# Performance work log

Hardware: AMD Instinct MI355X
Metric: run time of the kernel (lower is better)

## Reference

```python
import jax, jax.numpy as jnp
import numpy as np
import math

B, S, IN_DIM = 2048, 60, 211
D, H, L, DFF, NC = 192, 6, 3, 768, 35
DK = D // H


def make_pe(seq_len, d_model):
    pos = np.arange(seq_len)[:, None].astype(np.float32)
    div = np.exp(np.arange(0, d_model, 2).astype(np.float32) * (-math.log(10000.0) / d_model))
    pe = np.zeros((seq_len, d_model), dtype=np.float32)
    pe[:, 0::2] = np.sin(pos * div)
    pe[:, 1::2] = np.cos(pos * div)
    return jnp.asarray(pe)


def setup_inputs() -> dict:
    key = jax.random.key(0)
    ks = jax.random.split(key, 24)
    r = lambda k, shape, fan: jax.random.normal(k, shape, jnp.float32) * (1.0 / np.sqrt(fan))
    inp = {
        'x': jax.random.normal(ks[0], (B, S, IN_DIM), jnp.float32),
        'W_in': r(ks[1], (IN_DIM, D), IN_DIM), 'b_in': jnp.zeros((D,), jnp.float32),
        'pe': make_pe(S, D),
        'Wq': r(ks[2], (L, D, D), D), 'bq': jnp.zeros((L, D), jnp.float32),
        'Wk': r(ks[3], (L, D, D), D), 'bk': jnp.zeros((L, D), jnp.float32),
        'Wv': r(ks[4], (L, D, D), D), 'bv': jnp.zeros((L, D), jnp.float32),
        'Wo': r(ks[5], (L, D, D), D), 'bo': jnp.zeros((L, D), jnp.float32),
        'W1': r(ks[6], (L, D, DFF), D), 'b1': jnp.zeros((L, DFF), jnp.float32),
        'W2': r(ks[7], (L, DFF, D), DFF), 'b2': jnp.zeros((L, D), jnp.float32),
        'g1': jnp.ones((L, D), jnp.float32), 'be1': jnp.zeros((L, D), jnp.float32),
        'g2': jnp.ones((L, D), jnp.float32), 'be2': jnp.zeros((L, D), jnp.float32),
        'Wc1': r(ks[8], (D, D // 2), D), 'bc1': jnp.zeros((D // 2,), jnp.float32),
        'Wc2': r(ks[9], (D // 2, NC), D // 2), 'bc2': jnp.zeros((NC,), jnp.float32),
    }
    return inp


def layer_norm(x, g, b, eps=1e-5):
    mu = jnp.mean(x, axis=-1, keepdims=True)
    var = jnp.mean((x - mu) ** 2, axis=-1, keepdims=True)
    return (x - mu) * jax.lax.rsqrt(var + eps) * g + b


def mha(x, Wq, bq, Wk, bk, Wv, bv, Wo, bo):
    Bs, Ss, _ = x.shape
    q = (x @ Wq + bq).reshape(Bs, Ss, H, DK)
    k = (x @ Wk + bk).reshape(Bs, Ss, H, DK)
    v = (x @ Wv + bv).reshape(Bs, Ss, H, DK)
    scores = jnp.einsum('bqhd,bkhd->bhqk', q, k) / jnp.sqrt(jnp.float32(DK))
    attn = jax.nn.softmax(scores, axis=-1)
    ctx = jnp.einsum('bhqk,bkhd->bqhd', attn, v).reshape(Bs, Ss, D)
    return ctx @ Wo + bo


def encoder_layer(x, Wq, bq, Wk, bk, Wv, bv, Wo, bo, W1, b1, W2, b2, g1, be1, g2, be2):
    attn_out = mha(x, Wq, bq, Wk, bk, Wv, bv, Wo, bo)
    x = layer_norm(x + attn_out, g1, be1)
    ff = jax.nn.gelu(x @ W1 + b1, approximate=False) @ W2 + b2
    return layer_norm(x + ff, g2, be2)


def reference(x, W_in, b_in, pe, Wq, bq, Wk, bk, Wv, bv, Wo, bo,
              W1, b1, W2, b2, g1, be1, g2, be2, Wc1, bc1, Wc2, bc2):
    h = x @ W_in + b_in + pe  # [B,S,D]
    for l in range(L):
        h = encoder_layer(h, Wq[l], bq[l], Wk[l], bk[l], Wv[l], bv[l], Wo[l], bo[l],
                          W1[l], b1[l], W2[l], b2[l], g1[l], be1[l], g2[l], be2[l])
    hidden = jax.nn.gelu(h @ Wc1 + bc1, approximate=False)
    return hidden @ Wc2 + bc2  # [B,S,NC]
```

## Files before the change

kernel.cpp:

```cpp
#include <hip/hip_runtime.h>
#include <cmath>

#define B_   2048
#define S_   60
#define NTOK (B_*S_)
#define IND_ 211
#define D_   192
#define H_   6
#define DK_  32
#define L_   3
#define DFF_ 768
#define NC_  35
#define DH_  96

typedef unsigned short us_t;
typedef us_t us8 __attribute__((ext_vector_type(8)));
typedef us_t us4 __attribute__((ext_vector_type(4)));
typedef short sh8 __attribute__((ext_vector_type(8)));
typedef float f4 __attribute__((ext_vector_type(4)));

#define MFMA(a, b, cc) __builtin_amdgcn_mfma_f32_16x16x32_bf16((a), (b), (cc), 0, 0, 0)
#define ZACC(A, M, N) \
    for (int _i = 0; _i < (M); ++_i) \
        for (int _j = 0; _j < (N); ++_j) { \
            A[_i][_j][0] = 0.f; A[_i][_j][1] = 0.f; A[_i][_j][2] = 0.f; A[_i][_j][3] = 0.f; }
#define ZACC1(A, N) \
    for (int _j = 0; _j < (N); ++_j) { \
        A[_j][0] = 0.f; A[_j][1] = 0.f; A[_j][2] = 0.f; A[_j][3] = 0.f; }

__device__ __forceinline__ float bf2f(us_t u) {
    union { unsigned int i; float f; } v; v.i = ((unsigned int)u) << 16; return v.f;
}
__device__ __forceinline__ us_t f2bf(float f) {
    union { float f; unsigned int i; } v; v.f = f;
    unsigned int r = v.i + 0x7fffu + ((v.i >> 16) & 1u);
    return (us_t)(r >> 16);
}
__device__ __forceinline__ float gelu_f(float v) {
    float u = v * (0.7978845608f + 0.0356774081f * v * v);
    float e = __expf(2.f * u);
    float t = 1.f - 2.f / (e + 1.f);
    return 0.5f * v * (1.f + t);
}
__device__ __forceinline__ void gld16(const us_t* g, us_t* s) {
    __builtin_amdgcn_global_load_lds(
        (const __attribute__((address_space(1))) unsigned int*)(g),
        (__attribute__((address_space(3))) unsigned int*)(s), 16, 0, 0);
}

__global__ void prep_t(const float* __restrict__ in, us_t* __restrict__ out,
                       int K, int Kpad, int N)
{
    int e = blockIdx.x * 256 + threadIdx.x;
    if (e >= N * Kpad) return;
    int n = e / Kpad, kp = e % Kpad;
    out[e] = (kp < K) ? f2bf(in[(size_t)kp * N + n]) : (us_t)0;
}

__global__ void prep_ff(const float* __restrict__ W1, const float* __restrict__ W2,
                        us_t* __restrict__ WT)
{
    int e = blockIdx.x * 256 + threadIdx.x;
    if (e >= L_ * 48 * 6144) return;
    int l = e / (48 * 6144), r = e % (48 * 6144);
    int t = r / 6144, q = r % 6144;
    int col = q >> 5, kk = q & 31;
    int cb = t / 12, ph = (t / 6) & 1, s = t % 6;
    us_t v;
    if (!ph) v = f2bf(W1[((size_t)l * D_ + s * 32 + kk) * DFF_ + cb * 192 + col]);
    else     v = f2bf(W2[((size_t)l * DFF_ + cb * 192 + s * 32 + kk) * D_ + col]);
    WT[e] = v;
}

__global__ __launch_bounds__(256) void inp_mfma(
    const float* __restrict__ x, const us_t* __restrict__ Wint,
    const float* __restrict__ b_in, const float* __restrict__ pe,
    us_t* __restrict__ h)
{
    __shared__ __align__(16) char smem[29696 + 27648];
    us_t* Xs = (us_t*)smem;
    us_t* Ws = (us_t*)(smem + 29696);
    const int tid = threadIdx.x;
    const int lane = tid & 63, wid = tid >> 6;
    const int g = lane >> 4, c = lane & 15;
    const int wr = wid >> 1, wc = wid & 1;
    const int row0 = blockIdx.x * 64;

    for (int e = tid; e < 64 * 224; e += 256) {
        int tok = e / 224, kp = e % 224;
        float v = (kp < IND_) ? x[(size_t)(row0 + tok) * IND_ + kp] : 0.f;
        Xs[tok * 232 + kp] = f2bf(v);
    }

    f4 acc[2][6];
    ZACC(acc, 2, 6);
    for (int pc = 0; pc < 4; ++pc) {
        __syncthreads();
        const int nk = (pc < 3) ? 64 : 32;
        const int per = nk / 8;
        for (int e = tid; e < 192 * per; e += 256) {
            int rw = e / per, v = e % per;
            *(us8*)&Ws[rw * 72 + v * 8] =
                *(const us8*)&Wint[(size_t)rw * 224 + pc * 64 + v * 8];
        }
        __syncthreads();
        for (int kk = 0; kk < nk / 32; ++kk) {
            const int ka = pc * 64 + kk * 32 + g * 8;
            const int kw = kk * 32 + g * 8;
            sh8 a0 = *(const sh8*)&Xs[(32 * wr + c) * 232 + ka];
            sh8 a1 = *(const sh8*)&Xs[(32 * wr + 16 + c) * 232 + ka];
            #pragma unroll
            for (int ni = 0; ni < 6; ++ni) {
                sh8 bf = *(const sh8*)&Ws[(96 * wc + 16 * ni + c) * 72 + kw];
                acc[0][ni] = MFMA(a0, bf, acc[0][ni]);
                acc[1][ni] = MFMA(a1, bf, acc[1][ni]);
            }
        }
    }
    #pragma unroll
    for (int ni = 0; ni < 6; ++ni) {
        const int col = 96 * wc + 16 * ni + c;
        const float bv = b_in[col];
        #pragma unroll
        for (int mi = 0; mi < 2; ++mi)
            #pragma unroll
            for (int r = 0; r < 4; ++r) {
                int tokg = row0 + 32 * wr + 16 * mi + 4 * g + r;
                int s = tokg % S_;
                float val = acc[mi][ni][r] + bv + pe[(size_t)s * D_ + col];
                h[(size_t)tokg * D_ + col] = f2bf(val);
            }
    }
}

__global__ __launch_bounds__(512) void qkv_attn_wo(
    us_t* __restrict__ h,
    const us_t* __restrict__ Wqt, const us_t* __restrict__ Wkt,
    const us_t* __restrict__ Wvt, const us_t* __restrict__ Wot,
    const float* __restrict__ bq, const float* __restrict__ bk,
    const float* __restrict__ bv, const float* __restrict__ bo,
    const float* __restrict__ g1, const float* __restrict__ be1)
{
    __shared__ __align__(16) char smem[157696];
    us_t* Xs = (us_t*)smem;
    us_t* Qs = (us_t*)(smem + 25600);
    us_t* Ks = (us_t*)(smem + 51200);
    us_t* Vt = (us_t*)(smem + 76800);
    us_t* Ws = (us_t*)(smem + 104448);
    us_t* P0 = (us_t*)(smem + 104448);
    us_t* P1 = (us_t*)(smem + 113664);
    us_t* Cx = (us_t*)(smem + 132096);
    float* eL = (float*)(smem + 51200);

    const int tid = threadIdx.x;
    const int lane = tid & 63, wid = tid >> 6;
    const int g = lane >> 4, c = lane & 15;
    const int wr = wid >> 2, wc = wid & 3;
    us_t* hb = h + (size_t)blockIdx.x * (S_ * D_);

    for (int e = tid; e < 1536; e += 512) {
        int tok = e / 24, v = e % 24;
        us8 u = {0, 0, 0, 0, 0, 0, 0, 0};
        if (tok < S_) u = *(const us8*)&hb[(size_t)tok * D_ + v * 8];
        *(us8*)&Xs[tok * 200 + v * 8] = u;
    }

    for (int m = 0; m < 3; ++m) {
        const us_t* Wt = (m == 0) ? Wqt : (m == 1) ? Wkt : Wvt;
        const float* bb = (m == 0) ? bq : (m == 1) ? bk : bv;
        f4 acc[2][3];
        ZACC(acc, 2, 3);
        for (int pc = 0; pc < 3; ++pc) {
            __syncthreads();
            for (int e = tid; e < 1536; e += 512) {
                int rw = e >> 3, v = e & 7;
                *(us8*)&Ws[rw * 72 + v * 8] =
                    *(const us8*)&Wt[(size_t)rw * 192 + pc * 64 + v * 8];
            }
            __syncthreads();
            #pragma unroll
            for (int kk = 0; kk < 2; ++kk) {
                const int ka = pc * 64 + kk * 32 + g * 8;
                const int kw = kk * 32 + g * 8;
                sh8 a0 = *(const sh8*)&Xs[(32 * wr + c) * 200 + ka];
                sh8 a1 = *(const sh8*)&Xs[(32 * wr + 16 + c) * 200 + ka];
                #pragma unroll
                for (int ni = 0; ni < 3; ++ni) {
                    sh8 bf = *(const sh8*)&Ws[(48 * wc + 16 * ni + c) * 72 + kw];
                    acc[0][ni] = MFMA(a0, bf, acc[0][ni]);
                    acc[1][ni] = MFMA(a1, bf, acc[1][ni]);
                }
            }
        }
        #pragma unroll
        for (int ni = 0; ni < 3; ++ni) {
            const int col = 48 * wc + 16 * ni + c;
            const float bval = bb[col];
            #pragma unroll
            for (int mi = 0; mi < 2; ++mi)
                #pragma unroll
                for (int r = 0; r < 4; ++r) {
                    int tok = 32 * wr + 16 * mi + 4 * g + r;
                    us_t o = f2bf(acc[mi][ni][r] + bval);
                    if (m == 0)      Qs[tok * 200 + col] = o;
                    else if (m == 1) Ks[tok * 200 + col] = o;
                    else             Vt[col * 72 + tok] = o;
                }
        }
    }
    __syncthreads();

    const int hgrp = wid & 3;
    const int hsel = wid >> 2;
    for (int rr = 0; rr < 3; ++rr) {
        const int hh = 2 * rr + hsel;
        us_t* Pb = hsel ? P1 : P0;
        f4 sc[4];
        ZACC1(sc, 4);
        {
            const int ka = 32 * hh + g * 8;
            sh8 aq = *(const sh8*)&Qs[(16 * hgrp + c) * 200 + ka];
            #pragma unroll
            for (int ni = 0; ni < 4; ++ni) {
                sh8 bk8 = *(const sh8*)&Ks[(16 * ni + c) * 200 + ka];
                sc[ni] = MFMA(aq, bk8, sc[ni]);
            }
        }
        #pragma unroll
        for (int r = 0; r < 4; ++r) {
            float mx = -1e30f;
            #pragma unroll
            for (int ni = 0; ni < 4; ++ni) {
                float v = sc[ni][r] * 0.17677669529663687f;
                if (16 * ni + c >= S_) v = -1e30f;
                sc[ni][r] = v;
                mx = fmaxf(mx, v);
            }
            mx = fmaxf(mx, __shfl_xor(mx, 1));
            mx = fmaxf(mx, __shfl_xor(mx, 2));
            mx = fmaxf(mx, __shfl_xor(mx, 4));
            mx = fmaxf(mx, __shfl_xor(mx, 8));
            float sum = 0.f;
            #pragma unroll
            for (int ni = 0; ni < 4; ++ni) {
                float e = __expf(sc[ni][r] - mx);
                sc[ni][r] = e; sum += e;
            }
            sum += __shfl_xor(sum, 1);
            sum += __shfl_xor(sum, 2);
            sum += __shfl_xor(sum, 4);
            sum += __shfl_xor(sum, 8);
            const float inv = 1.f / sum;
            #pragma unroll
            for (int ni = 0; ni < 4; ++ni)
                Pb[(16 * hgrp + 4 * g + r) * 72 + 16 * ni + c] = f2bf(sc[ni][r] * inv);
        }
        __syncthreads();
        f4 ov[2];
        ZACC1(ov, 2);
        #pragma unroll
        for (int kk = 0; kk < 2; ++kk) {
            sh8 ap = *(const sh8*)&Pb[(16 * hgrp + c) * 72 + kk * 32 + g * 8];
            #pragma unroll
            for (int n2 = 0; n2 < 2; ++n2) {
                sh8 bv8 = *(const sh8*)&Vt[(32 * hh + 16 * n2 + c) * 72 + kk * 32 + g * 8];
                ov[n2] = MFMA(ap, bv8, ov[n2]);
            }
        }
        #pragma unroll
        for (int n2 = 0; n2 < 2; ++n2)
            #pragma unroll
            for (int r = 0; r < 4; ++r)
                Cx[(16 * hgrp + 4 * g + r) * 200 + 32 * hh + 16 * n2 + c] = f2bf(ov[n2][r]);
        __syncthreads();
    }

    f4 aw[2][3];
    ZACC(aw, 2, 3);
    for (int pc = 0; pc < 3; ++pc) {
        __syncthreads();
        for (int e = tid; e < 1536; e += 512) {
            int rw = e >> 3, v = e & 7;
            *(us8*)&Ws[rw * 72 + v * 8] =
                *(const us8*)&Wot[(size_t)rw * 192 + pc * 64 + v * 8];
        }
        __syncthreads();
        #pragma unroll
        for (int kk = 0; kk < 2; ++kk) {
            const int ka = pc * 64 + kk * 32 + g * 8;
            const int kw = kk * 32 + g * 8;
            sh8 a0 = *(const sh8*)&Cx[(32 * wr + c) * 200 + ka];
            sh8 a1 = *(const sh8*)&Cx[(32 * wr + 16 + c) * 200 + ka];
            #pragma unroll
            for (int ni = 0; ni < 3; ++ni) {
                sh8 bf = *(const sh8*)&Ws[(48 * wc + 16 * ni + c) * 72 + kw];
                aw[0][ni] = MFMA(a0, bf, aw[0][ni]);
                aw[1][ni] = MFMA(a1, bf, aw[1][ni]);
            }
        }
    }
    __syncthreads();
    #pragma unroll
    for (int ni = 0; ni < 3; ++ni) {
        const int col = 48 * wc + 16 * ni + c;
        const float bov = bo[col];
        #pragma unroll
        for (int mi = 0; mi < 2; ++mi)
            #pragma unroll
            for (int r = 0; r < 4; ++r) {
                int tok = 32 * wr + 16 * mi + 4 * g + r;
                eL[tok * 200 + col] = aw[mi][ni][r] + bov + bf2f(Xs[tok * 200 + col]);
            }
    }
    __syncthreads();
    {
        const int tok = tid >> 3, t8 = tid & 7;
        float vals[24], sum = 0.f, ssq = 0.f;
        #pragma unroll
        for (int jv = 0; jv < 6; ++jv) {
            float4 v4 = *(const float4*)&eL[tok * 200 + t8 * 24 + jv * 4];
            vals[jv*4+0] = v4.x; vals[jv*4+1] = v4.y; vals[jv*4+2] = v4.z; vals[jv*4+3] = v4.w;
            sum += v4.x + v4.y + v4.z + v4.w;
            ssq += v4.x*v4.x + v4.y*v4.y + v4.z*v4.z + v4.w*v4.w;
        }
        sum += __shfl_xor(sum, 1); sum += __shfl_xor(sum, 2); sum += __shfl_xor(sum, 4);
        ssq += __shfl_xor(ssq, 1); ssq += __shfl_xor(ssq, 2); ssq += __shfl_xor(ssq, 4);
        const float mean = sum * (1.f / D_);
        const float var  = ssq * (1.f / D_) - mean * mean;
        const float rstd = rsqrtf(var + 1e-5f);
        if (tok < S_) {
            #pragma unroll
            for (int jv = 0; jv < 6; ++jv) {
                us4 o4;
                #pragma unroll
                for (int j = 0; j < 4; ++j) {
                    int col = t8 * 24 + jv * 4 + j;
                    o4[j] = f2bf((vals[jv*4+j] - mean) * rstd * g1[col] + be1[col]);
                }
                *(us4*)&hb[(size_t)tok * D_ + t8 * 24 + jv * 4] = o4;
            }
        }
    }
}

__global__ __launch_bounds__(512) void ff_mfma(
    us_t* __restrict__ hio,
    const us_t* __restrict__ WT, const float* __restrict__ b1,
    const float* __restrict__ b2,
    const float* __restrict__ gamma, const float* __restrict__ beta)
{
    __shared__ __align__(16) char smem[76800];
    us_t* Xs  = (us_t*)smem;
    us_t* Ts  = (us_t*)(smem + 25600);
    us_t* Wsb = (us_t*)(smem + 51200);
    float* Sm = (float*)(smem + 75776);

    const int tid = threadIdx.x;
    const int lane = tid & 63, wid = tid >> 6;
    const int g = lane >> 4, c = lane & 15;
    const int wr = wid >> 1;
    const int wc = wid & 1;
    const int row0 = blockIdx.x * 64;

    auto stage = [&](int t) {
        const us_t* src = WT + (size_t)t * 6144;
        us_t* dst = Wsb + (t & 1) * 6144;
        for (int i = wid; i < 12; i += 8)
            gld16(src + i * 512 + lane * 8, dst + i * 512);
    };

    for (int e = tid; e < 1536; e += 512) {
        int tok = e / 24, v = e % 24;
        *(us8*)&Xs[tok * 200 + v * 8] = *(const us8*)&hio[(size_t)(row0 + tok) * D_ + v * 8];
    }
    stage(0);
    __syncthreads();

    f4 acc1[6], acc2[6];
    ZACC1(acc2, 6);
    for (int t = 0; t < 48; ++t) {
        const int s = t % 6, ph = (t / 6) & 1, cb = t / 12;
        if (t < 47) stage(t + 1);
        const us_t* W = Wsb + (t & 1) * 6144;
        if (!ph) {
            if (s == 0) ZACC1(acc1, 6);
            sh8 xb = *(const sh8*)&Xs[(16 * wr + c) * 200 + s * 32 + g * 8];
            #pragma unroll
            for (int ni = 0; ni < 6; ++ni) {
                sh8 wa = *(const sh8*)&W[(96 * wc + 16 * ni + c) * 32 + g * 8];
                acc1[ni] = MFMA(wa, xb, acc1[ni]);
            }
            if (s == 5) {
                #pragma unroll
                for (int ni = 0; ni < 6; ++ni) {
                    const int d0 = 96 * wc + 16 * ni + 4 * g;
                    us4 o4;
                    #pragma unroll
                    for (int r = 0; r < 4; ++r)
                        o4[r] = f2bf(gelu_f(acc1[ni][r] + b1[cb * 192 + d0 + r]));
                    *(us4*)&Ts[(16 * wr + c) * 200 + d0] = o4;
                }
            }
        } else {
            sh8 tb = *(const sh8*)&Ts[(16 * wr + c) * 200 + s * 32 + g * 8];
            #pragma unroll
            for (int ni = 0; ni < 6; ++ni) {
                sh8 wa = *(const sh8*)&W[(96 * wc + 16 * ni + c) * 32 + g * 8];
                acc2[ni] = MFMA(wa, tb, acc2[ni]);
            }
        }
        __syncthreads();
    }

    float v[6][4];
    float sum = 0.f, ssq = 0.f;
    const int xrow = (16 * wr + c) * 200;
    #pragma unroll
    for (int ni = 0; ni < 6; ++ni)
        #pragma unroll
        for (int r = 0; r < 4; ++r) {
            const int dcol = 96 * wc + 16 * ni + 4 * g + r;
            float val = acc2[ni][r] + b2[dcol] + bf2f(Xs[xrow + dcol]);
            v[ni][r] = val; sum += val; ssq += val * val;
        }
    sum += __shfl_xor(sum, 16); sum += __shfl_xor(sum, 32);
    ssq += __shfl_xor(ssq, 16); ssq += __shfl_xor(ssq, 32);
    if (g == 0) {
        Sm[((0 * 2 + wc) * 4 + wr) * 16 + c] = sum;
        Sm[((1 * 2 + wc) * 4 + wr) * 16 + c] = ssq;
    }
    __syncthreads();
    sum += Sm[((0 * 2 + (1 - wc)) * 4 + wr) * 16 + c];
    ssq += Sm[((1 * 2 + (1 - wc)) * 4 + wr) * 16 + c];
    const float mean = sum * (1.f / D_);
    const float var  = ssq * (1.f / D_) - mean * mean;
    const float rstd = rsqrtf(var + 1e-5f);
    us_t* orow = hio + (size_t)(row0 + 16 * wr + c) * D_;
    #pragma unroll
    for (int ni = 0; ni < 6; ++ni) {
        const int d0 = 96 * wc + 16 * ni + 4 * g;
        us4 o4;
        #pragma unroll
        for (int r = 0; r < 4; ++r)
            o4[r] = f2bf((v[ni][r] - mean) * rstd * gamma[d0 + r] + beta[d0 + r]);
        *(us4*)&orow[d0] = o4;
    }
}

__global__ __launch_bounds__(256) void clf1_mfma(
    const us_t* __restrict__ h, const us_t* __restrict__ Wc1t,
    const float* __restrict__ bc1, us_t* __restrict__ hid)
{
    __shared__ __align__(16) char smem[25600 + 13824];
    us_t* Xs = (us_t*)smem;
    us_t* Ws = (us_t*)(smem + 25600);
    const int tid = threadIdx.x;
    const int lane = tid & 63, wid = tid >> 6;
    const int g = lane >> 4, c = lane & 15;
    const int wr = wid >> 1, wc = wid & 1;
    const int row0 = blockIdx.x * 64;

    for (int e = tid; e < 1536; e += 256) {
        int tok = e / 24, v = e % 24;
        *(us8*)&Xs[tok * 200 + v * 8] = *(const us8*)&h[(size_t)(row0 + tok) * D_ + v * 8];
    }
    f4 acc[2][3];
    ZACC(acc, 2, 3);
    for (int pc = 0; pc < 3; ++pc) {
        __syncthreads();
        for (int e = tid; e < 768; e += 256) {
            int rw = e >> 3, v = e & 7;
            *(us8*)&Ws[rw * 72 + v * 8] =
                *(const us8*)&Wc1t[(size_t)rw * 192 + pc * 64 + v * 8];
        }
        __syncthreads();
        #pragma unroll
        for (int kk = 0; kk < 2; ++kk) {
            const int ka = pc * 64 + kk * 32 + g * 8;
            const int kw = kk * 32 + g * 8;
            sh8 a0 = *(const sh8*)&Xs[(32 * wr + c) * 200 + ka];
            sh8 a1 = *(const sh8*)&Xs[(32 * wr + 16 + c) * 200 + ka];
            #pragma unroll
            for (int ni = 0; ni < 3; ++ni) {
                sh8 bf = *(const sh8*)&Ws[(48 * wc + 16 * ni + c) * 72 + kw];
                acc[0][ni] = MFMA(a0, bf, acc[0][ni]);
                acc[1][ni] = MFMA(a1, bf, acc[1][ni]);
            }
        }
    }
    #pragma unroll
    for (int ni = 0; ni < 3; ++ni) {
        const int col = 48 * wc + 16 * ni + c;
        const float bv = bc1[col];
        #pragma unroll
        for (int mi = 0; mi < 2; ++mi)
            #pragma unroll
            for (int r = 0; r < 4; ++r) {
                int tok = row0 + 32 * wr + 16 * mi + 4 * g + r;
                hid[(size_t)tok * DH_ + col] = f2bf(gelu_f(acc[mi][ni][r] + bv));
            }
    }
}

__global__ __launch_bounds__(256) void clf2_kernel(
    const us_t* __restrict__ hid, const float* __restrict__ Wc2,
    const float* __restrict__ bc2, float* __restrict__ out)
{
    __shared__ us_t Hs[64 * 104];
    __shared__ float Wl[DH_ * NC_];
    __shared__ float bl[NC_];
    const int tid = threadIdx.x;
    const int row0 = blockIdx.x * 64;
    for (int e = tid; e < 768; e += 256) {
        int tok = e / 12, v = e % 12;
        *(us8*)&Hs[tok * 104 + v * 8] = *(const us8*)&hid[(size_t)(row0 + tok) * DH_ + v * 8];
    }
    for (int e = tid; e < DH_ * NC_; e += 256) Wl[e] = Wc2[e];
    if (tid < NC_) bl[tid] = bc2[tid];
    __syncthreads();
    for (int e = tid; e < 64 * NC_; e += 256) {
        const int tok = e / NC_, col = e % NC_;
        float acc = bl[col];
        #pragma unroll 8
        for (int kk = 0; kk < DH_; ++kk)
            acc = fmaf(bf2f(Hs[tok * 104 + kk]), Wl[kk * NC_ + col], acc);
        out[(size_t)(row0 + tok) * NC_ + col] = acc;
    }
}

extern "C" void kernel_launch(void* const* d_in, const int* in_sizes, int n_in,
                              void* d_out, int out_size, void* d_ws, size_t ws_size,
                              hipStream_t stream)
{
    const float* x    = (const float*)d_in[0];
    const float* W_in = (const float*)d_in[1];
    const float* b_in = (const float*)d_in[2];
    const float* pe   = (const float*)d_in[3];
    const float* Wq   = (const float*)d_in[4];
    const float* bq   = (const float*)d_in[5];
    const float* Wk   = (const float*)d_in[6];
    const float* bk   = (const float*)d_in[7];
    const float* Wv   = (const float*)d_in[8];
    const float* bv   = (const float*)d_in[9];
    const float* Wo   = (const float*)d_in[10];
    const float* bo   = (const float*)d_in[11];
    const float* W1   = (const float*)d_in[12];
    const float* b1   = (const float*)d_in[13];
    const float* W2   = (const float*)d_in[14];
    const float* b2   = (const float*)d_in[15];
    const float* g1   = (const float*)d_in[16];
    const float* be1  = (const float*)d_in[17];
    const float* g2   = (const float*)d_in[18];
    const float* be2  = (const float*)d_in[19];
    const float* Wc1  = (const float*)d_in[20];
    const float* bc1  = (const float*)d_in[21];
    const float* Wc2  = (const float*)d_in[22];
    const float* bc2  = (const float*)d_in[23];
    float* outp = (float*)d_out;

    us_t* h    = (us_t*)d_ws;
    us_t* hid  = h + (size_t)NTOK * D_;
    us_t* Wint = hid + (size_t)NTOK * DH_;
    us_t* Wqt  = Wint + 192 * 224;
    us_t* Wkt  = Wqt + 3 * 36864;
    us_t* Wvt  = Wkt + 3 * 36864;
    us_t* Wot  = Wvt + 3 * 36864;
    us_t* WT   = Wot + 3 * 36864;
    us_t* Wc1t = WT + (size_t)L_ * 48 * 6144;

    prep_t<<<168, 256, 0, stream>>>(W_in, Wint, IND_, 224, D_);
    for (int l = 0; l < L_; ++l) {
        prep_t<<<144, 256, 0, stream>>>(Wq + (size_t)l * 36864, Wqt + (size_t)l * 36864, 192, 192, 192);
        prep_t<<<144, 256, 0, stream>>>(Wk + (size_t)l * 36864, Wkt + (size_t)l * 36864, 192, 192, 192);
        prep_t<<<144, 256, 0, stream>>>(Wv + (size_t)l * 36864, Wvt + (size_t)l * 36864, 192, 192, 192);
        prep_t<<<144, 256, 0, stream>>>(Wo + (size_t)l * 36864, Wot + (size_t)l * 36864, 192, 192, 192);
    }
    prep_ff<<<(L_ * 48 * 6144 + 255) / 256, 256, 0, stream>>>(W1, W2, WT);
    prep_t<<<72, 256, 0, stream>>>(Wc1, Wc1t, 192, 192, DH_);

    inp_mfma<<<NTOK / 64, 256, 0, stream>>>(x, Wint, b_in, pe, h);

    for (int l = 0; l < L_; ++l) {
        qkv_attn_wo<<<B_, 512, 0, stream>>>(
            h,
            Wqt + (size_t)l * 36864, Wkt + (size_t)l * 36864,
            Wvt + (size_t)l * 36864, Wot + (size_t)l * 36864,
            bq + l * D_, bk + l * D_, bv + l * D_, bo + l * D_,
            g1 + l * D_, be1 + l * D_);
        ff_mfma<<<NTOK / 64, 512, 0, stream>>>(
            h, WT + (size_t)l * 48 * 6144, b1 + l * DFF_, b2 + l * D_,
            g2 + l * D_, be2 + l * D_);
    }

    clf1_mfma<<<NTOK / 64, 256, 0, stream>>>(h, Wc1t, bc1, hid);
    clf2_kernel<<<NTOK / 64, 256, 0, stream>>>(hid, Wc2, bc2, outp);
}
```

Before: 1.349 ms.

## Retile FF kernel warps to 2x4 and pad weight tiles to 40-element rows

```diff
diff --git a/kernel.cpp b/kernel.cpp
--- a/kernel.cpp
+++ b/kernel.cpp
@@ -61,14 +61,16 @@
                         us_t* __restrict__ WT)
 {
     int e = blockIdx.x * 256 + threadIdx.x;
-    if (e >= L_ * 48 * 6144) return;
-    int l = e / (48 * 6144), r = e % (48 * 6144);
-    int t = r / 6144, q = r % 6144;
-    int col = q >> 5, kk = q & 31;
+    if (e >= L_ * 48 * 7680) return;
+    int l = e / (48 * 7680), r = e % (48 * 7680);
+    int t = r / 7680, q = r % 7680;
+    int col = q / 40, kk = q % 40;
     int cb = t / 12, ph = (t / 6) & 1, s = t % 6;
-    us_t v;
-    if (!ph) v = f2bf(W1[((size_t)l * D_ + s * 32 + kk) * DFF_ + cb * 192 + col]);
-    else     v = f2bf(W2[((size_t)l * DFF_ + cb * 192 + s * 32 + kk) * D_ + col]);
+    us_t v = 0;
+    if (kk < 32) {
+        if (!ph) v = f2bf(W1[((size_t)l * D_ + s * 32 + kk) * DFF_ + cb * 192 + col]);
+        else     v = f2bf(W2[((size_t)l * DFF_ + cb * 192 + s * 32 + kk) * D_ + col]);
+    }
     WT[e] = v;
 }
 
@@ -349,23 +351,23 @@
     const float* __restrict__ b2,
     const float* __restrict__ gamma, const float* __restrict__ beta)
 {
-    __shared__ __align__(16) char smem[76800];
+    __shared__ __align__(16) char smem[81920];
     us_t* Xs  = (us_t*)smem;
     us_t* Ts  = (us_t*)(smem + 25600);
     us_t* Wsb = (us_t*)(smem + 51200);
-    float* Sm = (float*)(smem + 75776);
+    float* Sm = (float*)(smem + 25600);
 
     const int tid = threadIdx.x;
     const int lane = tid & 63, wid = tid >> 6;
     const int g = lane >> 4, c = lane & 15;
-    const int wr = wid >> 1;
-    const int wc = wid & 1;
+    const int wr = wid >> 2;
+    const int wc = wid & 3;
     const int row0 = blockIdx.x * 64;
 
     auto stage = [&](int t) {
-        const us_t* src = WT + (size_t)t * 6144;
-        us_t* dst = Wsb + (t & 1) * 6144;
-        for (int i = wid; i < 12; i += 8)
+        const us_t* src = WT + (size_t)t * 7680;
+        us_t* dst = Wsb + (t & 1) * 7680;
+        for (int i = wid; i < 15; i += 8)
             gld16(src + i * 512 + lane * 8, dst + i * 512);
     };
 
@@ -376,74 +378,100 @@
     stage(0);
     __syncthreads();
 
-    f4 acc1[6], acc2[6];
-    ZACC1(acc2, 6);
+    f4 acc1[2][3], acc2[2][3];
+    ZACC(acc2, 2, 3);
     for (int t = 0; t < 48; ++t) {
         const int s = t % 6, ph = (t / 6) & 1, cb = t / 12;
         if (t < 47) stage(t + 1);
-        const us_t* W = Wsb + (t & 1) * 6144;
+        const us_t* W = Wsb + (t & 1) * 7680;
         if (!ph) {
-            if (s == 0) ZACC1(acc1, 6);
-            sh8 xb = *(const sh8*)&Xs[(16 * wr + c) * 200 + s * 32 + g * 8];
-            #pragma unroll
-            for (int ni = 0; ni < 6; ++ni) {
-                sh8 wa = *(const sh8*)&W[(96 * wc + 16 * ni + c) * 32 + g * 8];
-                acc1[ni] = MFMA(wa, xb, acc1[ni]);
+            if (s == 0) ZACC(acc1, 2, 3);
+            sh8 xb0 = *(const sh8*)&Xs[(32 * wr + c) * 200 + s * 32 + g * 8];
+            sh8 xb1 = *(const sh8*)&Xs[(32 * wr + 16 + c) * 200 + s * 32 + g * 8];
+            #pragma unroll
+            for (int ni = 0; ni < 3; ++ni) {
+                sh8 wa = *(const sh8*)&W[(48 * wc + 16 * ni + c) * 40 + g * 8];
+                acc1[0][ni] = MFMA(wa, xb0, acc1[0][ni]);
+                acc1[1][ni] = MFMA(wa, xb1, acc1[1][ni]);
             }
             if (s == 5) {
                 #pragma unroll
-                for (int ni = 0; ni < 6; ++ni) {
-                    const int d0 = 96 * wc + 16 * ni + 4 * g;
-                    us4 o4;
+                for (int mi = 0; mi < 2; ++mi)
                     #pragma unroll
-                    for (int r = 0; r < 4; ++r)
-                        o4[r] = f2bf(gelu_f(acc1[ni][r] + b1[cb * 192 + d0 + r]));
-                    *(us4*)&Ts[(16 * wr + c) * 200 + d0] = o4;
-                }
+                    for (int ni = 0; ni < 3; ++ni) {
+                        const int d0 = 48 * wc + 16 * ni + 4 * g;
+                        const int tok = 32 * wr + 16 * mi + c;
+                        us4 o4;
+                        #pragma unroll
+                        for (int r = 0; r < 4; ++r)
+                            o4[r] = f2bf(gelu_f(acc1[mi][ni][r] + b1[cb * 192 + d0 + r]));
+                        *(us4*)&Ts[tok * 200 + d0] = o4;
+                    }
             }
         } else {
-            sh8 tb = *(const sh8*)&Ts[(16 * wr + c) * 200 + s * 32 + g * 8];
-            #pragma unroll
-            for (int ni = 0; ni < 6; ++ni) {
-                sh8 wa = *(const sh8*)&W[(96 * wc + 16 * ni + c) * 32 + g * 8];
-                acc2[ni] = MFMA(wa, tb, acc2[ni]);
-            }
-        }
-        __syncthreads();
-    }
-
-    float v[6][4];
-    float sum = 0.f, ssq = 0.f;
-    const int xrow = (16 * wr + c) * 200;
+            sh8 tb0 = *(const sh8*)&Ts[(32 * wr + c) * 200 + s * 32 + g * 8];
+            sh8 tb1 = *(const sh8*)&Ts[(32 * wr + 16 + c) * 200 + s * 32 + g * 8];
+            #pragma unroll
+            for (int ni = 0; ni < 3; ++ni) {
+                sh8 wa = *(const sh8*)&W[(48 * wc + 16 * ni + c) * 40 + g * 8];
+                acc2[0][ni] = MFMA(wa, tb0, acc2[0][ni]);
+                acc2[1][ni] = MFMA(wa, tb1, acc2[1][ni]);
+            }
+        }
+        __syncthreads();
+    }
+
+    float v[2][3][4];
+    float sum[2] = {0.f, 0.f}, ssq[2] = {0.f, 0.f};
     #pragma unroll
-    for (int ni = 0; ni < 6; ++ni)
-        #pragma unroll
-        for (int r = 0; r < 4; ++r) {
-            const int dcol = 96 * wc + 16 * ni + 4 * g + r;
-            float val = acc2[ni][r] + b2[dcol] + bf2f(Xs[xrow + dcol]);
-            v[ni][r] = val; sum += val; ssq += val * val;
-        }
-    sum += __shfl_xor(sum, 16); sum += __shfl_xor(sum, 32);
-    ssq += __shfl_xor(ssq, 16); ssq += __shfl_xor(ssq, 32);
+    for (int mi = 0; mi < 2; ++mi) {
+        const int tok = 32 * wr + 16 * mi + c;
+        #pragma unroll
+        for (int ni = 0; ni < 3; ++ni) {
+            const int d0 = 48 * wc + 16 * ni + 4 * g;
+            us4 rv = *(const us4*)&Xs[tok * 200 + d0];
+            #pragma unroll
+            for (int r = 0; r < 4; ++r) {
+                float val = acc2[mi][ni][r] + b2[d0 + r] + bf2f(rv[r]);
+                v[mi][ni][r] = val; sum[mi] += val; ssq[mi] += val * val;
+            }
+        }
+    }
+    #pragma unroll
+    for (int mi = 0; mi < 2; ++mi) {
+        sum[mi] += __shfl_xor(sum[mi], 16); sum[mi] += __shfl_xor(sum[mi], 32);
+        ssq[mi] += __shfl_xor(ssq[mi], 16); ssq[mi] += __shfl_xor(ssq[mi], 32);
+    }
     if (g == 0) {
-        Sm[((0 * 2 + wc) * 4 + wr) * 16 + c] = sum;
-        Sm[((1 * 2 + wc) * 4 + wr) * 16 + c] = ssq;
+        #pragma unroll
+        for (int mi = 0; mi < 2; ++mi) {
+            Sm[(((0 * 4 + wc) * 2 + wr) * 2 + mi) * 16 + c] = sum[mi];
+            Sm[(((1 * 4 + wc) * 2 + wr) * 2 + mi) * 16 + c] = ssq[mi];
+        }
     }
     __syncthreads();
-    sum += Sm[((0 * 2 + (1 - wc)) * 4 + wr) * 16 + c];
-    ssq += Sm[((1 * 2 + (1 - wc)) * 4 + wr) * 16 + c];
-    const float mean = sum * (1.f / D_);
-    const float var  = ssq * (1.f / D_) - mean * mean;
-    const float rstd = rsqrtf(var + 1e-5f);
-    us_t* orow = hio + (size_t)(row0 + 16 * wr + c) * D_;
     #pragma unroll
-    for (int ni = 0; ni < 6; ++ni) {
-        const int d0 = 96 * wc + 16 * ni + 4 * g;
-        us4 o4;
-        #pragma unroll
-        for (int r = 0; r < 4; ++r)
-            o4[r] = f2bf((v[ni][r] - mean) * rstd * gamma[d0 + r] + beta[d0 + r]);
-        *(us4*)&orow[d0] = o4;
+    for (int mi = 0; mi < 2; ++mi) {
+        float st = 0.f, qt = 0.f;
+        #pragma unroll
+        for (int w = 0; w < 4; ++w) {
+            st += Sm[(((0 * 4 + w) * 2 + wr) * 2 + mi) * 16 + c];
+            qt += Sm[(((1 * 4 + w) * 2 + wr) * 2 + mi) * 16 + c];
+        }
+        const float mean = st * (1.f / D_);
+        const float var  = qt * (1.f / D_) - mean * mean;
+        const float rstd = rsqrtf(var + 1e-5f);
+        const int tok = 32 * wr + 16 * mi + c;
+        us_t* orow = hio + (size_t)(row0 + tok) * D_;
+        #pragma unroll
+        for (int ni = 0; ni < 3; ++ni) {
+            const int d0 = 48 * wc + 16 * ni + 4 * g;
+            us4 o4;
+            #pragma unroll
+            for (int r = 0; r < 4; ++r)
+                o4[r] = f2bf((v[mi][ni][r] - mean) * rstd * gamma[d0 + r] + beta[d0 + r]);
+            *(us4*)&orow[d0] = o4;
+        }
     }
 }
 
@@ -566,7 +594,7 @@
     us_t* Wvt  = Wkt + 3 * 36864;
     us_t* Wot  = Wvt + 3 * 36864;
     us_t* WT   = Wot + 3 * 36864;
-    us_t* Wc1t = WT + (size_t)L_ * 48 * 6144;
+    us_t* Wc1t = WT + (size_t)L_ * 48 * 7680;
 
     prep_t<<<168, 256, 0, stream>>>(W_in, Wint, IND_, 224, D_);
     for (int l = 0; l < L_; ++l) {
@@ -575,7 +603,7 @@
         prep_t<<<144, 256, 0, stream>>>(Wv + (size_t)l * 36864, Wvt + (size_t)l * 36864, 192, 192, 192);
         prep_t<<<144, 256, 0, stream>>>(Wo + (size_t)l * 36864, Wot + (size_t)l * 36864, 192, 192, 192);
     }
-    prep_ff<<<(L_ * 48 * 6144 + 255) / 256, 256, 0, stream>>>(W1, W2, WT);
+    prep_ff<<<(L_ * 48 * 7680 + 255) / 256, 256, 0, stream>>>(W1, W2, WT);
     prep_t<<<72, 256, 0, stream>>>(Wc1, Wc1t, 192, 192, DH_);
 
     inp_mfma<<<NTOK / 64, 256, 0, stream>>>(x, Wint, b_in, pe, h);
@@ -588,7 +616,7 @@
             bq + l * D_, bk + l * D_, bv + l * D_, bo + l * D_,
             g1 + l * D_, be1 + l * D_);
         ff_mfma<<<NTOK / 64, 512, 0, stream>>>(
-            h, WT + (size_t)l * 48 * 6144, b1 + l * DFF_, b2 + l * D_,
+            h, WT + (size_t)l * 48 * 7680, b1 + l * DFF_, b2 + l * D_,
             g2 + l * D_, be2 + l * D_);
     }
 
```

New measurement: 1.265 ms. -6.2%, faster.

## Restructure FFN kernel to keep activations in registers with triple-buffered padded weights

Applied to the files above, without the earlier changes.

```diff
diff --git a/kernel.cpp b/kernel.cpp
--- a/kernel.cpp
+++ b/kernel.cpp
@@ -18,6 +18,7 @@
 typedef us_t us4 __attribute__((ext_vector_type(4)));
 typedef short sh8 __attribute__((ext_vector_type(8)));
 typedef float f4 __attribute__((ext_vector_type(4)));
+typedef int i4v __attribute__((ext_vector_type(4)));
 
 #define MFMA(a, b, cc) __builtin_amdgcn_mfma_f32_16x16x32_bf16((a), (b), (cc), 0, 0, 0)
 #define ZACC(A, M, N) \
@@ -61,14 +62,18 @@
                         us_t* __restrict__ WT)
 {
     int e = blockIdx.x * 256 + threadIdx.x;
-    if (e >= L_ * 48 * 6144) return;
-    int l = e / (48 * 6144), r = e % (48 * 6144);
-    int t = r / 6144, q = r % 6144;
-    int col = q >> 5, kk = q & 31;
-    int cb = t / 12, ph = (t / 6) & 1, s = t % 6;
-    us_t v;
-    if (!ph) v = f2bf(W1[((size_t)l * D_ + s * 32 + kk) * DFF_ + cb * 192 + col]);
-    else     v = f2bf(W2[((size_t)l * DFF_ + cb * 192 + s * 32 + kk) * D_ + col]);
+    if (e >= L_ * 48 * 8192) return;
+    int l = e / (48 * 8192), r = e % (48 * 8192);
+    int t = r / 8192, q = r % 8192;
+    int cb = t / 12, p = t % 12, ph = p / 6, s = p % 6;
+    us_t v = 0;
+    if (q < 7680) {
+        int col = q / 40, kk = q % 40;
+        if (kk < 32) {
+            if (!ph) v = f2bf(W1[((size_t)l * D_ + s * 32 + kk) * DFF_ + cb * 192 + col]);
+            else     v = f2bf(W2[((size_t)l * DFF_ + cb * 192 + s * 32 + kk) * D_ + col]);
+        }
+    }
     WT[e] = v;
 }
 
@@ -349,100 +354,132 @@
     const float* __restrict__ b2,
     const float* __restrict__ gamma, const float* __restrict__ beta)
 {
-    __shared__ __align__(16) char smem[76800];
-    us_t* Xs  = (us_t*)smem;
-    us_t* Ts  = (us_t*)(smem + 25600);
-    us_t* Wsb = (us_t*)(smem + 51200);
-    float* Sm = (float*)(smem + 75776);
+    __shared__ __align__(16) us_t Wsb[3][8192];
 
     const int tid = threadIdx.x;
     const int lane = tid & 63, wid = tid >> 6;
     const int g = lane >> 4, c = lane & 15;
-    const int wr = wid >> 1;
-    const int wc = wid & 1;
-    const int row0 = blockIdx.x * 64;
-
-    auto stage = [&](int t) {
-        const us_t* src = WT + (size_t)t * 6144;
-        us_t* dst = Wsb + (t & 1) * 6144;
-        for (int i = wid; i < 12; i += 8)
-            gld16(src + i * 512 + lane * 8, dst + i * 512);
+    const int row0 = blockIdx.x * 128;
+    const int trow = row0 + 16 * wid + c;
+
+    auto stage = [&](int t, int slot) {
+        const us_t* src = WT + (size_t)t * 8192;
+        us_t* dst = &Wsb[slot][0];
+        #pragma unroll
+        for (int i = 0; i < 2; ++i)
+            gld16(src + (wid * 2 + i) * 512 + lane * 8, dst + (wid * 2 + i) * 512);
     };
 
-    for (int e = tid; e < 1536; e += 512) {
-        int tok = e / 24, v = e % 24;
-        *(us8*)&Xs[tok * 200 + v * 8] = *(const us8*)&hio[(size_t)(row0 + tok) * D_ + v * 8];
-    }
-    stage(0);
-    __syncthreads();
-
-    f4 acc1[6], acc2[6];
-    ZACC1(acc2, 6);
-    for (int t = 0; t < 48; ++t) {
-        const int s = t % 6, ph = (t / 6) & 1, cb = t / 12;
-        if (t < 47) stage(t + 1);
-        const us_t* W = Wsb + (t & 1) * 6144;
-        if (!ph) {
-            if (s == 0) ZACC1(acc1, 6);
-            sh8 xb = *(const sh8*)&Xs[(16 * wr + c) * 200 + s * 32 + g * 8];
-            #pragma unroll
-            for (int ni = 0; ni < 6; ++ni) {
-                sh8 wa = *(const sh8*)&W[(96 * wc + 16 * ni + c) * 32 + g * 8];
-                acc1[ni] = MFMA(wa, xb, acc1[ni]);
-            }
-            if (s == 5) {
+    stage(0, 0);
+    stage(1, 1);
+    sh8 Xf[6];
+    {
+        const us_t* hr = hio + (size_t)trow * D_;
+        #pragma unroll
+        for (int s = 0; s < 6; ++s)
+            Xf[s] = *(const sh8*)&hr[32 * s + 8 * g];
+    }
+    asm volatile("s_waitcnt vmcnt(2)" ::: "memory");
+    __builtin_amdgcn_s_barrier();
+
+    f4 acc1[12], acc2[12];
+    ZACC1(acc2, 12);
+    unsigned tp[12][2];
+
+    for (int cb = 0; cb < 4; ++cb) {
+        ZACC1(acc1, 12);
+        #pragma unroll
+        for (int p = 0; p < 12; ++p) {
+            const int t = cb * 12 + p;
+            const int s = p % 6;
+            const bool isff1 = (p < 6);
+            const bool dostage = (t + 2 < 48);
+            if (dostage) stage(t + 2, (p + 2) % 3);
+            const us_t* W = &Wsb[p % 3][0];
+
+            if (isff1) {
                 #pragma unroll
-                for (int ni = 0; ni < 6; ++ni) {
-                    const int d0 = 96 * wc + 16 * ni + 4 * g;
-                    us4 o4;
-                    #pragma unroll
-                    for (int r = 0; r < 4; ++r)
-                        o4[r] = f2bf(gelu_f(acc1[ni][r] + b1[cb * 192 + d0 + r]));
-                    *(us4*)&Ts[(16 * wr + c) * 200 + d0] = o4;
+                for (int ni = 0; ni < 12; ++ni) {
+                    sh8 wa = *(const sh8*)&W[(16 * ni + c) * 40 + 8 * g];
+                    acc1[ni] = MFMA(wa, Xf[s], acc1[ni]);
                 }
-            }
-        } else {
-            sh8 tb = *(const sh8*)&Ts[(16 * wr + c) * 200 + s * 32 + g * 8];
-            #pragma unroll
-            for (int ni = 0; ni < 6; ++ni) {
-                sh8 wa = *(const sh8*)&W[(96 * wc + 16 * ni + c) * 32 + g * 8];
-                acc2[ni] = MFMA(wa, tb, acc2[ni]);
-            }
-        }
-        __syncthreads();
-    }
-
-    float v[6][4];
+            } else {
+                unsigned P0 = tp[2 * s + (g >> 1)][0];
+                unsigned P1 = tp[2 * s + (g >> 1)][1];
+                unsigned Q0 = tp[2 * s + ((g >> 1) ^ 1)][0];
+                unsigned Q1 = tp[2 * s + ((g >> 1) ^ 1)][1];
+                unsigned r16_0 = (unsigned)__shfl_xor((int)P0, 16);
+                unsigned r16_1 = (unsigned)__shfl_xor((int)P1, 16);
+                unsigned r32_0 = (unsigned)__shfl_xor((int)Q0, 32);
+                unsigned r32_1 = (unsigned)__shfl_xor((int)Q1, 32);
+                unsigned r48_0 = (unsigned)__shfl_xor((int)Q0, 48);
+                unsigned r48_1 = (unsigned)__shfl_xor((int)Q1, 48);
+                unsigned a0, a1, d0, d1;
+                if (g == 0)      { a0 = P0;    a1 = P1;    d0 = r16_0; d1 = r16_1; }
+                else if (g == 1) { a0 = r48_0; a1 = r48_1; d0 = r32_0; d1 = r32_1; }
+                else if (g == 2) { a0 = r32_0; a1 = r32_1; d0 = r48_0; d1 = r48_1; }
+                else             { a0 = r16_0; a1 = r16_1; d0 = P0;    d1 = P1;    }
+                union { i4v u; sh8 s8; } cvt;
+                cvt.u[0] = (int)a0; cvt.u[1] = (int)a1; cvt.u[2] = (int)d0; cvt.u[3] = (int)d1;
+                sh8 Tf = cvt.s8;
+                #pragma unroll
+                for (int ni = 0; ni < 12; ++ni) {
+                    sh8 wa = *(const sh8*)&W[(16 * ni + c) * 40 + 8 * g];
+                    acc2[ni] = MFMA(wa, Tf, acc2[ni]);
+                }
+            }
+
+            if (isff1 && s == 5) {
+                #pragma unroll
+                for (int ni = 0; ni < 12; ++ni) {
+                    float4 bv = *(const float4*)&b1[cb * 192 + 16 * ni + 4 * g];
+                    float t0 = gelu_f(acc1[ni][0] + bv.x);
+                    float t1 = gelu_f(acc1[ni][1] + bv.y);
+                    float t2 = gelu_f(acc1[ni][2] + bv.z);
+                    float t3 = gelu_f(acc1[ni][3] + bv.w);
+                    tp[ni][0] = (unsigned)f2bf(t0) | ((unsigned)f2bf(t1) << 16);
+                    tp[ni][1] = (unsigned)f2bf(t2) | ((unsigned)f2bf(t3) << 16);
+                }
+                asm volatile("s_waitcnt vmcnt(0)" ::: "memory");
+            } else if (dostage) {
+                asm volatile("s_waitcnt vmcnt(2)" ::: "memory");
+            } else {
+                asm volatile("s_waitcnt vmcnt(0)" ::: "memory");
+            }
+            __builtin_amdgcn_s_barrier();
+        }
+    }
+
+    const us_t* hr = hio + (size_t)trow * D_;
+    float vv[12][4];
     float sum = 0.f, ssq = 0.f;
-    const int xrow = (16 * wr + c) * 200;
     #pragma unroll
-    for (int ni = 0; ni < 6; ++ni)
+    for (int ni = 0; ni < 12; ++ni) {
+        const int d0 = 16 * ni + 4 * g;
+        float4 b2v = *(const float4*)&b2[d0];
+        us4 rv = *(const us4*)&hr[d0];
         #pragma unroll
         for (int r = 0; r < 4; ++r) {
-            const int dcol = 96 * wc + 16 * ni + 4 * g + r;
-            float val = acc2[ni][r] + b2[dcol] + bf2f(Xs[xrow + dcol]);
-            v[ni][r] = val; sum += val; ssq += val * val;
-        }
+            float val = acc2[ni][r] + ((const float*)&b2v)[r] + bf2f(rv[r]);
+            vv[ni][r] = val; sum += val; ssq += val * val;
+        }
+    }
     sum += __shfl_xor(sum, 16); sum += __shfl_xor(sum, 32);
     ssq += __shfl_xor(ssq, 16); ssq += __shfl_xor(ssq, 32);
-    if (g == 0) {
-        Sm[((0 * 2 + wc) * 4 + wr) * 16 + c] = sum;
-        Sm[((1 * 2 + wc) * 4 + wr) * 16 + c] = ssq;
-    }
-    __syncthreads();
-    sum += Sm[((0 * 2 + (1 - wc)) * 4 + wr) * 16 + c];
-    ssq += Sm[((1 * 2 + (1 - wc)) * 4 + wr) * 16 + c];
     const float mean = sum * (1.f / D_);
     const float var  = ssq * (1.f / D_) - mean * mean;
     const float rstd = rsqrtf(var + 1e-5f);
-    us_t* orow = hio + (size_t)(row0 + 16 * wr + c) * D_;
+    us_t* orow = hio + (size_t)trow * D_;
     #pragma unroll
-    for (int ni = 0; ni < 6; ++ni) {
-        const int d0 = 96 * wc + 16 * ni + 4 * g;
+    for (int ni = 0; ni < 12; ++ni) {
+        const int d0 = 16 * ni + 4 * g;
+        float4 gv  = *(const float4*)&gamma[d0];
+        float4 bev = *(const float4*)&beta[d0];
         us4 o4;
-        #pragma unroll
-        for (int r = 0; r < 4; ++r)
-            o4[r] = f2bf((v[ni][r] - mean) * rstd * gamma[d0 + r] + beta[d0 + r]);
+        o4[0] = f2bf((vv[ni][0] - mean) * rstd * gv.x + bev.x);
+        o4[1] = f2bf((vv[ni][1] - mean) * rstd * gv.y + bev.y);
+        o4[2] = f2bf((vv[ni][2] - mean) * rstd * gv.z + bev.z);
+        o4[3] = f2bf((vv[ni][3] - mean) * rstd * gv.w + bev.w);
         *(us4*)&orow[d0] = o4;
     }
 }
@@ -566,7 +603,7 @@
     us_t* Wvt  = Wkt + 3 * 36864;
     us_t* Wot  = Wvt + 3 * 36864;
     us_t* WT   = Wot + 3 * 36864;
-    us_t* Wc1t = WT + (size_t)L_ * 48 * 6144;
+    us_t* Wc1t = WT + (size_t)L_ * 48 * 8192;
 
     prep_t<<<168, 256, 0, stream>>>(W_in, Wint, IND_, 224, D_);
     for (int l = 0; l < L_; ++l) {
@@ -575,7 +612,7 @@
         prep_t<<<144, 256, 0, stream>>>(Wv + (size_t)l * 36864, Wvt + (size_t)l * 36864, 192, 192, 192);
         prep_t<<<144, 256, 0, stream>>>(Wo + (size_t)l * 36864, Wot + (size_t)l * 36864, 192, 192, 192);
     }
-    prep_ff<<<(L_ * 48 * 6144 + 255) / 256, 256, 0, stream>>>(W1, W2, WT);
+    prep_ff<<<(L_ * 48 * 8192 + 255) / 256, 256, 0, stream>>>(W1, W2, WT);
     prep_t<<<72, 256, 0, stream>>>(Wc1, Wc1t, 192, 192, DH_);
 
     inp_mfma<<<NTOK / 64, 256, 0, stream>>>(x, Wint, b_in, pe, h);
@@ -587,8 +624,8 @@
             Wvt + (size_t)l * 36864, Wot + (size_t)l * 36864,
             bq + l * D_, bk + l * D_, bv + l * D_, bo + l * D_,
             g1 + l * D_, be1 + l * D_);
-        ff_mfma<<<NTOK / 64, 512, 0, stream>>>(
-            h, WT + (size_t)l * 48 * 6144, b1 + l * DFF_, b2 + l * D_,
+        ff_mfma<<<NTOK / 128, 512, 0, stream>>>(
+            h, WT + (size_t)l * 48 * 8192, b1 + l * DFF_, b2 + l * D_,
             g2 + l * D_, be2 + l * D_);
     }
 
```

Result: slower. 1.553 ms (+15.2%).
